# Kernel optimization log

Measured on AMD Instinct MI355X. Metric: run time of the kernel, lower is better.

Reference implementation:

```python
import jax, jax.numpy as jnp
import numpy as np

B, L, D = 4, 2048, 1024
H, HD = 16, 64
SCALE = 1.0 / np.sqrt(H).astype(np.float32)  # NOTE: source divides by sqrt(head_num), not sqrt(head_dim)
NEG = -10000000.0


def setup_inputs() -> dict:
    key = jax.random.key(0)
    ks = jax.random.split(key, 7)
    s = 1.0 / np.sqrt(D).astype(np.float32)
    return {
        "X": jax.random.normal(ks[0], (B, L, D), dtype=jnp.float32),
        "Wq": jax.random.normal(ks[1], (D, D), dtype=jnp.float32) * s,
        "bq": jnp.zeros((D,), dtype=jnp.float32),
        "Wk": jax.random.normal(ks[2], (D, D), dtype=jnp.float32) * s,
        "bk": jnp.zeros((D,), dtype=jnp.float32),
        "Wv": jax.random.normal(ks[3], (D, D), dtype=jnp.float32) * s,
        "bv": jnp.zeros((D,), dtype=jnp.float32),
    }


def _split_heads(x):
    # [B, L, D] -> [B, H, L, HD]
    return x.reshape(B, L, H, HD).transpose(0, 2, 1, 3)


def reference(X, Wq, bq, Wk, bk, Wv, bv):
    Q = _split_heads(X @ Wq.T + bq)
    K = _split_heads(X @ Wk.T + bk)
    V = _split_heads(X @ Wv.T + bv)
    logits = jnp.einsum('bhld,bhmd->bhlm', Q, K) * SCALE
    # causal mask: strictly-upper-triangular entries get a large negative additive bias
    mask = jnp.triu(jnp.full((L, L), NEG, dtype=logits.dtype), k=1)
    logits = logits + mask[None, None, :, :]
    w = jax.nn.softmax(logits, axis=-1)
    out = jnp.einsum('bhlm,bhmd->bhld', w, V)
    # combine heads: [B, H, L, HD] -> [B, L, D]
    return out.transpose(0, 2, 1, 3).reshape(B, L, H * HD)
```

## Files before the change

kernel.cpp:

```cpp
#include <hip/hip_runtime.h>
#include <hip/hip_bf16.h>

#define L_SEQ   2048
#define DMODEL  1024
#define NH      16
#define HD      64
#define MROWS   8192
#define QSC     0.360673760222f
#define NEG2    -2.0e7f

typedef float  f32x4 __attribute__((ext_vector_type(4)));
typedef short  s16x8 __attribute__((ext_vector_type(8)));

__device__ __forceinline__ unsigned short f2bf(float f) {
    union { float f; unsigned u; } v; v.f = f;
    unsigned r = (v.u + 0x7FFFu + ((v.u >> 16) & 1u)) >> 16;
    return (unsigned short)r;
}

__device__ __forceinline__ float fexp2(float x) {
#if __has_builtin(__builtin_amdgcn_exp2f)
    return __builtin_amdgcn_exp2f(x);
#else
    return __expf(x * 0.6931471805599453f);
#endif
}

__device__ __forceinline__ unsigned pk2(float a, float b) {
    union { float f; unsigned u; } ua, ub; ua.f = a; ub.f = b;
    return __builtin_amdgcn_perm(ub.u, ua.u, 0x07060302u);
}

__device__ __forceinline__ void gl_lds16(const void* g, void* l) {
    __builtin_amdgcn_global_load_lds(
        (const __attribute__((address_space(1))) unsigned int*)g,
        (__attribute__((address_space(3))) unsigned int*)l, 16, 0, 0);
}

__global__ __launch_bounds__(256) void cvt_all(const float* __restrict__ X,
                                               const float* __restrict__ W0,
                                               const float* __restrict__ W1,
                                               const float* __restrict__ W2,
                                               unsigned short* __restrict__ Xb,
                                               unsigned short* __restrict__ Wb) {
    const int bx = blockIdx.x, tid = threadIdx.x;
    const float* src; unsigned short* dst; int i;
    if (bx < 8192) {
        src = X; dst = Xb; i = bx * 256 + tid;
    } else {
        int r = bx - 8192; const int wsel = r >> 10; r &= 1023;
        src = (wsel == 0) ? W0 : (wsel == 1) ? W1 : W2;
        dst = Wb + (size_t)wsel * (DMODEL * DMODEL);
        i = r * 256 + tid;
    }
    float4 v = ((const float4*)src)[i];
    ushort4 o;
    o.x = f2bf(v.x); o.y = f2bf(v.y); o.z = f2bf(v.z); o.w = f2bf(v.w);
    ((ushort4*)dst)[i] = o;
}

__global__ __launch_bounds__(256, 2) void qkv_gemm(
        const unsigned short* __restrict__ Xb,
        const unsigned short* __restrict__ Wb,
        const float* __restrict__ bq, const float* __restrict__ bk_,
        const float* __restrict__ bv,
        unsigned short* __restrict__ Yb) {
    __shared__ unsigned short As[128 * 64];
    __shared__ unsigned short Bs[128 * 64];

    const int tid = threadIdx.x;
    const int w = tid >> 6, l = tid & 63, q = l >> 4, t = l & 15;
    const int mw = w >> 1, nw = w & 1;
    const int z = blockIdx.z;
    const int rowM0 = blockIdx.x * 128;
    const int colN0 = blockIdx.y * 128;

    const unsigned short* W = Wb + (size_t)z * (DMODEL * DMODEL);
    unsigned short* Y = Yb + (size_t)z * ((size_t)MROWS * DMODEL);
    const float* bias = (z == 0) ? bq : (z == 1) ? bk_ : bv;
    const float osc = (z == 0) ? QSC : 1.0f;

    f32x4 acc[4][4] = {};

    const int srow8 = l >> 3;
    const int sch_g = ((l & 7) ^ srow8) * 8;

    const int coff0 = ((q) ^ (t & 7)) * 8;
    const int coff1 = ((4 + q) ^ (t & 7)) * 8;

    for (int k0 = 0; k0 < DMODEL; k0 += 64) {
        #pragma unroll
        for (int r = 0; r < 4; ++r) {
            const int row = w * 32 + r * 8;
            gl_lds16(Xb + (size_t)(rowM0 + row + srow8) * DMODEL + k0 + sch_g, As + row * 64);
            gl_lds16(W  + (size_t)(colN0 + row + srow8) * DMODEL + k0 + sch_g, Bs + row * 64);
        }
        __syncthreads();
        #pragma unroll
        for (int ks = 0; ks < 2; ++ks) {
            const int co = ks ? coff1 : coff0;
            s16x8 a[4], b[4];
            #pragma unroll
            for (int i = 0; i < 4; ++i) {
                a[i] = *(const s16x8*)&As[(mw * 64 + i * 16 + t) * 64 + co];
                b[i] = *(const s16x8*)&Bs[(nw * 64 + i * 16 + t) * 64 + co];
            }
            #pragma unroll
            for (int in = 0; in < 4; ++in)
                #pragma unroll
                for (int jm = 0; jm < 4; ++jm)
                    acc[in][jm] = __builtin_amdgcn_mfma_f32_16x16x32_bf16(b[in], a[jm], acc[in][jm], 0, 0, 0);
        }
        __syncthreads();
    }

    const int bb = rowM0 >> 11;
    #pragma unroll
    for (int in = 0; in < 4; ++in) {
        const int ncol = colN0 + nw * 64 + in * 16 + q * 4;
        const int hh = ncol >> 6, hd = ncol & 63;
        const float4 b4 = *(const float4*)&bias[ncol];
        unsigned short* Yh = Y + ((size_t)(bb * NH + hh) * L_SEQ) * HD + hd;
        #pragma unroll
        for (int jm = 0; jm < 4; ++jm) {
            const int sl = (rowM0 & 2047) + mw * 64 + jm * 16 + t;
            unsigned lo = ((unsigned)f2bf((acc[in][jm][0] + b4.x) * osc)) |
                          ((unsigned)f2bf((acc[in][jm][1] + b4.y) * osc) << 16);
            unsigned hi = ((unsigned)f2bf((acc[in][jm][2] + b4.z) * osc)) |
                          ((unsigned)f2bf((acc[in][jm][3] + b4.w) * osc) << 16);
            uint2 o; o.x = lo; o.y = hi;
            *(uint2*)&Yh[(size_t)sl * HD] = o;
        }
    }
}

__global__ __launch_bounds__(256, 2) void attn_fwd(
        const unsigned short* __restrict__ Qb,
        const unsigned short* __restrict__ Kb,
        const unsigned short* __restrict__ Vb,
        float* __restrict__ out) {
    __shared__ __align__(16) unsigned short Ks[2][64 * 64];
    __shared__ __align__(16) unsigned short Vt[2][64 * 72];

    const int tid = threadIdx.x;
    const int w = tid >> 6, l = tid & 63, q = l >> 4, t = l & 15;

    const int lin = blockIdx.x;
    const int xcd = lin & 7;
    const int bhg = (lin >> 3) & 7;
    const int qt  = 15 - (lin >> 6);
    const int bh  = bhg * 8 + xcd;
    const int b = bh >> 4, h = bh & 15;
    const size_t base = (size_t)bh * (L_SEQ * HD);

    const int Q0 = qt * 128;
    const int n = 2 * qt + 2;
    const int m_min = Q0 + w * 32;

    const int d8 = tid >> 5, jp = tid & 31;
    const int vslot = ((jp >> 4) << 5) | (((jp >> 1) & 3) << 3) | (((jp >> 3) & 1) << 2) | ((jp & 1) << 1);
    const int krow_in = l >> 3;
    const int kchunk_g = (l & 7) ^ krow_in;

    int kaddr[4][2], vaddr[4][2];
    #pragma unroll
    for (int nt = 0; nt < 4; ++nt)
        #pragma unroll
        for (int ks = 0; ks < 2; ++ks) {
            kaddr[nt][ks] = (nt * 16 + t) * 64 + (((ks * 4 + q) ^ (t & 7)) * 8);
            vaddr[nt][ks] = (nt * 16 + t) * 72 + ks * 32 + q * 8;
        }

    s16x8 vone;
    #pragma unroll
    for (int i = 0; i < 8; ++i) vone[i] = (short)0x3F80;

    auto issueK = [&](int jbase, unsigned short* dst) {
        #pragma unroll
        for (int r = 0; r < 2; ++r) {
            const int rb = r * 4 + w;
            gl_lds16(Kb + base + (size_t)(jbase + rb * 8 + krow_in) * HD + kchunk_g * 8,
                     dst + rb * 512);
        }
    };
    auto loadV = [&](int jbase, uint4& a, uint4& bb2) {
        const unsigned short* vp = Vb + base + (size_t)(jbase + 2 * jp) * HD + d8 * 8;
        a   = *(const uint4*)vp;
        bb2 = *(const uint4*)(vp + HD);
    };
    auto writeV = [&](const uint4& a, const uint4& bb2, unsigned short* dst) {
        const unsigned* u0 = (const unsigned*)&a;
        const unsigned* u1 = (const unsigned*)&bb2;
        #pragma unroll
        for (int i = 0; i < 4; ++i) {
            *(unsigned*)&dst[(d8 * 8 + 2 * i)     * 72 + vslot] = __builtin_amdgcn_perm(u1[i], u0[i], 0x05040100u);
            *(unsigned*)&dst[(d8 * 8 + 2 * i + 1) * 72 + vslot] = __builtin_amdgcn_perm(u1[i], u0[i], 0x07060302u);
        }
    };

    s16x8 qfrag[2][2];
    #pragma unroll
    for (int g = 0; g < 2; ++g) {
        const unsigned short* qp = Qb + base + (size_t)(Q0 + w * 32 + g * 16 + t) * HD + q * 8;
        qfrag[g][0] = *(const s16x8*)(qp);
        qfrag[g][1] = *(const s16x8*)(qp + 32);
    }

    f32x4 accO[2][4] = {};
    f32x4 accL[2] = {};

    issueK(0, Ks[0]);
    {
        uint4 a, bb2; loadV(0, a, bb2); writeV(a, bb2, Vt[0]);
    }
    __syncthreads();

    for (int c = 0; c < n; ++c) {
        const int cur = c & 1;
        const int jbase = c * 64;
        const bool pf = (c + 1 < n);
        uint4 va, vb2;
        if (pf) { issueK(jbase + 64, Ks[cur ^ 1]); loadV(jbase + 64, va, vb2); }

        if (jbase < m_min + 32) {
            const unsigned short* KsB = Ks[cur];
            const unsigned short* VtB = Vt[cur];
            unsigned Pu[2][8];
            #pragma unroll
            for (int g = 0; g < 2; ++g) {
                f32x4 st[4];
                #pragma unroll
                for (int nt = 0; nt < 4; ++nt) {
                    f32x4 zz = {};
                    #pragma unroll
                    for (int ks = 0; ks < 2; ++ks) {
                        s16x8 ak = *(const s16x8*)&KsB[kaddr[nt][ks]];
                        zz = __builtin_amdgcn_mfma_f32_16x16x32_bf16(ak, qfrag[g][ks], zz, 0, 0, 0);
                    }
                    st[nt] = zz;
                }
                if (jbase + 63 > m_min) {
                    const int ma = m_min + g * 16 + t;
                    #pragma unroll
                    for (int nt = 0; nt < 4; ++nt)
                        #pragma unroll
                        for (int r = 0; r < 4; ++r)
                            if (jbase + nt * 16 + q * 4 + r > ma) st[nt][r] += NEG2;
                }
                #pragma unroll
                for (int nt = 0; nt < 4; ++nt) {
                    float p0 = fexp2(st[nt][0]);
                    float p1 = fexp2(st[nt][1]);
                    float p2 = fexp2(st[nt][2]);
                    float p3 = fexp2(st[nt][3]);
                    Pu[g][2 * nt]     = pk2(p0, p1);
                    Pu[g][2 * nt + 1] = pk2(p2, p3);
                }
            }
            #pragma unroll
            for (int ks = 0; ks < 2; ++ks) {
                #pragma unroll
                for (int nt = 0; nt < 4; ++nt) {
                    s16x8 vb = *(const s16x8*)&VtB[vaddr[nt][ks]];
                    #pragma unroll
                    for (int g = 0; g < 2; ++g)
                        accO[g][nt] = __builtin_amdgcn_mfma_f32_16x16x32_bf16(
                            *(const s16x8*)&Pu[g][ks * 4], vb, accO[g][nt], 0, 0, 0);
                }
                #pragma unroll
                for (int g = 0; g < 2; ++g)
                    accL[g] = __builtin_amdgcn_mfma_f32_16x16x32_bf16(
                        *(const s16x8*)&Pu[g][ks * 4], vone, accL[g], 0, 0, 0);
            }
        }

        if (pf) writeV(va, vb2, Vt[cur ^ 1]);
        __syncthreads();
    }

    #pragma unroll
    for (int g = 0; g < 2; ++g) {
        f32x4 inv;
        #pragma unroll
        for (int r = 0; r < 4; ++r) inv[r] = 1.0f / accL[g][r];
        #pragma unroll
        for (int nt = 0; nt < 4; ++nt) {
            #pragma unroll
            for (int r = 0; r < 4; ++r) {
                const int row = Q0 + w * 32 + g * 16 + q * 4 + r;
                out[((size_t)(b * L_SEQ + row)) * DMODEL + h * HD + nt * 16 + t] =
                    accO[g][nt][r] * inv[r];
            }
        }
    }
}

extern "C" void kernel_launch(void* const* d_in, const int* in_sizes, int n_in,
                              void* d_out, int out_size, void* d_ws, size_t ws_size,
                              hipStream_t stream) {
    const float* X  = (const float*)d_in[0];
    const float* Wq = (const float*)d_in[1];
    const float* bq = (const float*)d_in[2];
    const float* Wk = (const float*)d_in[3];
    const float* bk = (const float*)d_in[4];
    const float* Wv = (const float*)d_in[5];
    const float* bv = (const float*)d_in[6];
    float* out = (float*)d_out;

    unsigned short* Xb = (unsigned short*)d_ws;
    unsigned short* Wb = Xb + (size_t)MROWS * DMODEL;
    unsigned short* Yb = Wb + (size_t)3 * DMODEL * DMODEL;

    cvt_all<<<8192 + 3 * 1024, 256, 0, stream>>>(X, Wq, Wk, Wv, Xb, Wb);

    qkv_gemm<<<dim3(64, 8, 3), 256, 0, stream>>>(Xb, Wb, bq, bk, bv, Yb);

    const size_t hs = (size_t)MROWS * DMODEL;
    attn_fwd<<<1024, 256, 0, stream>>>(Yb, Yb + hs, Yb + 2 * hs, out);
}
```

Before: 209.6 us.

## Store V pre-transposed from projection and load it via direct-to-LDS async copies

The QKV projection epilogue now writes V (z==2) transposed as [bh][d][L], with the key positions permuted to match the MFMA P-operand order, and without the output scale. The attention kernel then loads V tiles with the same gl_lds16 swizzled async path used for K, and reads them with K's addresses. This removes the per-tile register round-trip, perm shuffles and padded LDS stores for V, and shrinks the LDS buffer. The cost is scattered 2-byte global stores in the projection epilogue, which write strided and are poorly coalesced.

```diff
diff --git a/kernel.cpp b/kernel.cpp
--- a/kernel.cpp
+++ b/kernel.cpp
@@ -115,21 +115,41 @@
     }
 
     const int bb = rowM0 >> 11;
-    #pragma unroll
-    for (int in = 0; in < 4; ++in) {
-        const int ncol = colN0 + nw * 64 + in * 16 + q * 4;
-        const int hh = ncol >> 6, hd = ncol & 63;
-        const float4 b4 = *(const float4*)&bias[ncol];
-        unsigned short* Yh = Y + ((size_t)(bb * NH + hh) * L_SEQ) * HD + hd;
-        #pragma unroll
-        for (int jm = 0; jm < 4; ++jm) {
-            const int sl = (rowM0 & 2047) + mw * 64 + jm * 16 + t;
-            unsigned lo = ((unsigned)f2bf((acc[in][jm][0] + b4.x) * osc)) |
-                          ((unsigned)f2bf((acc[in][jm][1] + b4.y) * osc) << 16);
-            unsigned hi = ((unsigned)f2bf((acc[in][jm][2] + b4.z) * osc)) |
-                          ((unsigned)f2bf((acc[in][jm][3] + b4.w) * osc) << 16);
-            uint2 o; o.x = lo; o.y = hi;
-            *(uint2*)&Yh[(size_t)sl * HD] = o;
+    if (z < 2) {
+        #pragma unroll
+        for (int in = 0; in < 4; ++in) {
+            const int ncol = colN0 + nw * 64 + in * 16 + q * 4;
+            const int hh = ncol >> 6, hd = ncol & 63;
+            const float4 b4 = *(const float4*)&bias[ncol];
+            unsigned short* Yh = Y + ((size_t)(bb * NH + hh) * L_SEQ) * HD + hd;
+            #pragma unroll
+            for (int jm = 0; jm < 4; ++jm) {
+                const int sl = (rowM0 & 2047) + mw * 64 + jm * 16 + t;
+                unsigned lo = ((unsigned)f2bf((acc[in][jm][0] + b4.x) * osc)) |
+                              ((unsigned)f2bf((acc[in][jm][1] + b4.y) * osc) << 16);
+                unsigned hi = ((unsigned)f2bf((acc[in][jm][2] + b4.z) * osc)) |
+                              ((unsigned)f2bf((acc[in][jm][3] + b4.w) * osc) << 16);
+                uint2 o; o.x = lo; o.y = hi;
+                *(uint2*)&Yh[(size_t)sl * HD] = o;
+            }
+        }
+    } else {
+        const int g64 = (rowM0 & 2047) + mw * 64;
+        #pragma unroll
+        for (int in = 0; in < 4; ++in) {
+            const int ncol = colN0 + nw * 64 + in * 16 + q * 4;
+            const int hh = ncol >> 6;
+            const int d0 = in * 16 + q * 4;
+            const float4 b4 = *(const float4*)&bias[ncol];
+            unsigned short* Yh = Y + (size_t)(bb * NH + hh) * (L_SEQ * HD);
+            #pragma unroll
+            for (int jm = 0; jm < 4; ++jm) {
+                const int slot = g64 + ((jm >> 1) << 5) + ((t >> 2) << 3) + ((jm & 1) << 2) + (t & 3);
+                Yh[(size_t)(d0 + 0) * L_SEQ + slot] = f2bf(acc[in][jm][0] + b4.x);
+                Yh[(size_t)(d0 + 1) * L_SEQ + slot] = f2bf(acc[in][jm][1] + b4.y);
+                Yh[(size_t)(d0 + 2) * L_SEQ + slot] = f2bf(acc[in][jm][2] + b4.z);
+                Yh[(size_t)(d0 + 3) * L_SEQ + slot] = f2bf(acc[in][jm][3] + b4.w);
+            }
         }
     }
 }
@@ -137,10 +157,10 @@
 __global__ __launch_bounds__(256, 2) void attn_fwd(
         const unsigned short* __restrict__ Qb,
         const unsigned short* __restrict__ Kb,
-        const unsigned short* __restrict__ Vb,
+        const unsigned short* __restrict__ VTb,
         float* __restrict__ out) {
     __shared__ __align__(16) unsigned short Ks[2][64 * 64];
-    __shared__ __align__(16) unsigned short Vt[2][64 * 72];
+    __shared__ __align__(16) unsigned short Vt[2][64 * 64];
 
     const int tid = threadIdx.x;
     const int w = tid >> 6, l = tid & 63, q = l >> 4, t = l & 15;
@@ -157,19 +177,15 @@
     const int n = 2 * qt + 2;
     const int m_min = Q0 + w * 32;
 
-    const int d8 = tid >> 5, jp = tid & 31;
-    const int vslot = ((jp >> 4) << 5) | (((jp >> 1) & 3) << 3) | (((jp >> 3) & 1) << 2) | ((jp & 1) << 1);
     const int krow_in = l >> 3;
     const int kchunk_g = (l & 7) ^ krow_in;
 
-    int kaddr[4][2], vaddr[4][2];
+    int kaddr[4][2];
     #pragma unroll
     for (int nt = 0; nt < 4; ++nt)
         #pragma unroll
-        for (int ks = 0; ks < 2; ++ks) {
+        for (int ks = 0; ks < 2; ++ks)
             kaddr[nt][ks] = (nt * 16 + t) * 64 + (((ks * 4 + q) ^ (t & 7)) * 8);
-            vaddr[nt][ks] = (nt * 16 + t) * 72 + ks * 32 + q * 8;
-        }
 
     s16x8 vone;
     #pragma unroll
@@ -183,18 +199,12 @@
                      dst + rb * 512);
         }
     };
-    auto loadV = [&](int jbase, uint4& a, uint4& bb2) {
-        const unsigned short* vp = Vb + base + (size_t)(jbase + 2 * jp) * HD + d8 * 8;
-        a   = *(const uint4*)vp;
-        bb2 = *(const uint4*)(vp + HD);
-    };
-    auto writeV = [&](const uint4& a, const uint4& bb2, unsigned short* dst) {
-        const unsigned* u0 = (const unsigned*)&a;
-        const unsigned* u1 = (const unsigned*)&bb2;
-        #pragma unroll
-        for (int i = 0; i < 4; ++i) {
-            *(unsigned*)&dst[(d8 * 8 + 2 * i)     * 72 + vslot] = __builtin_amdgcn_perm(u1[i], u0[i], 0x05040100u);
-            *(unsigned*)&dst[(d8 * 8 + 2 * i + 1) * 72 + vslot] = __builtin_amdgcn_perm(u1[i], u0[i], 0x07060302u);
+    auto issueV = [&](int jbase, unsigned short* dst) {
+        #pragma unroll
+        for (int r = 0; r < 2; ++r) {
+            const int rb = r * 4 + w;
+            gl_lds16(VTb + base + (size_t)(rb * 8 + krow_in) * L_SEQ + jbase + kchunk_g * 8,
+                     dst + rb * 512);
         }
     };
 
@@ -210,17 +220,13 @@
     f32x4 accL[2] = {};
 
     issueK(0, Ks[0]);
-    {
-        uint4 a, bb2; loadV(0, a, bb2); writeV(a, bb2, Vt[0]);
-    }
+    issueV(0, Vt[0]);
     __syncthreads();
 
     for (int c = 0; c < n; ++c) {
         const int cur = c & 1;
         const int jbase = c * 64;
-        const bool pf = (c + 1 < n);
-        uint4 va, vb2;
-        if (pf) { issueK(jbase + 64, Ks[cur ^ 1]); loadV(jbase + 64, va, vb2); }
+        if (c + 1 < n) { issueK(jbase + 64, Ks[cur ^ 1]); issueV(jbase + 64, Vt[cur ^ 1]); }
 
         if (jbase < m_min + 32) {
             const unsigned short* KsB = Ks[cur];
@@ -261,7 +267,7 @@
             for (int ks = 0; ks < 2; ++ks) {
                 #pragma unroll
                 for (int nt = 0; nt < 4; ++nt) {
-                    s16x8 vb = *(const s16x8*)&VtB[vaddr[nt][ks]];
+                    s16x8 vb = *(const s16x8*)&VtB[kaddr[nt][ks]];
                     #pragma unroll
                     for (int g = 0; g < 2; ++g)
                         accO[g][nt] = __builtin_amdgcn_mfma_f32_16x16x32_bf16(
@@ -274,7 +280,6 @@
             }
         }
 
-        if (pf) writeV(va, vb2, Vt[cur ^ 1]);
         __syncthreads();
     }
 
```

Result: faster. 192.0 us (-8.4%).
